# Optimization experiments

Hardware: AMD Instinct MI355X
Metric: run time of the kernel (lower is better)

The kernel has to match this reference:

```python
import jax, jax.numpy as jnp
import numpy as np

HID = 256; H2 = 512; EMB = 128
B, K, NR, LR, LQ, NQ = 16, 4, 5, 100, 60, 5
VOCAB, EXTRA = 50000, 100
EPS = 1e-12


def setup_inputs() -> dict:
    key = jax.random.key(0)
    ks = jax.random.split(key, 32)
    n = lambda k, s, sc=1.0: jax.random.normal(k, s, jnp.float32) * sc
    W = 0.02
    return {
        'y_t': n(ks[0], (B, EMB)),
        'h0': n(ks[1], (B, HID)),
        'c0': n(ks[2], (B, HID)),
        'c_t_0': n(ks[3], (B, H2)),
        'o_m': n(ks[4], (B, H2 + EMB)),
        'h_q': n(ks[5], (B, NQ, LQ, H2)),
        'q_mask': jnp.ones((B, LQ), jnp.float32),
        'q_a': n(ks[6], (B, NQ, EMB)),
        'h_r': n(ks[7], (B, K, NR, LR, H2)),
        'r_mask': jnp.ones((B, K, LR), jnp.float32),
        'r_a': n(ks[8], (B, K, NR, EMB)),
        'r_o': n(ks[9], (B, K, NR, EMB)),
        'qr_cov': jnp.zeros((B, LQ + K * LR), jnp.float32),
        'extra_zeros': jnp.zeros((B, EXTRA), jnp.float32),
        'xc_w': n(ks[10], (EMB, EMB + H2), W),
        'xc_b': jnp.zeros((EMB,), jnp.float32),
        'w_ih': n(ks[11], (4 * HID, EMB), W),
        'w_hh': n(ks[12], (4 * HID, HID), W),
        'b_ih': jnp.zeros((4 * HID,), jnp.float32),
        'b_hh': jnp.zeros((4 * HID,), jnp.float32),
        'dsq_w': n(ks[13], (H2, EMB), W),
        'dsa_w': n(ks[14], (H2 + EMB, EMB), W),
        'dso_w': n(ks[15], (2 * H2 + EMB, EMB), W),
        'U_w': n(ks[16], (H2, H2), W),
        'Wc_w': n(ks[17], (H2,), W),
        'Ws_w': n(ks[18], (H2, H2), W),
        'Wqr_w': n(ks[19], (H2, H2), W),
        'Wqr_b': jnp.zeros((H2,), jnp.float32),
        'Vr_w': n(ks[20], (H2,), W),
        'pg_w': n(ks[21], (2 * H2,), W),
        'pg_b': jnp.zeros((), jnp.float32),
        'pv1_w': n(ks[22], (H2, 2 * H2), W),
        'pv1_b': jnp.zeros((H2,), jnp.float32),
        'pv2_w': n(ks[23], (VOCAB, H2), W),
        'pv2_b': jnp.zeros((VOCAB,), jnp.float32),
        'batch_extend_vocab': jax.random.randint(ks[24], (B, LQ + K * LR), 0, VOCAB + EXTRA),
        'step': 1,
    }


def dynamic_select(W, s_t, h_s, s_a):
    # s_t: [b, D]; h_s: [b, n, l, h]; s_a: [b, n, e]; bilinear -> tanh -> sum-normalize
    w = jnp.tanh(jnp.einsum('bd,de,bne->bn', s_t, W, s_a))
    w = w / (w.sum(axis=1, keepdims=True) + EPS)
    w_h_s = jnp.einsum('bn,bnlh->blh', w, h_s)
    w_a = jnp.einsum('bn,bne->be', w, s_a)
    return w_h_s, w_a


def decoder_attention(U_w, Wc_w, Ws_w, Wqr_w, Wqr_b, Vr_w, h_q, q_mask, h_r, r_mask, s_t, qr_cov):
    # h_q: [b,l_q,h]; h_r: [b,k,l_r,h]
    b, l_q, h = h_q.shape
    k, l_r = h_r.shape[1], h_r.shape[2]
    qU = h_q @ U_w.T                                        # [b,l_q,h]
    U = jnp.tanh(jnp.einsum('bqh,bkrh->bkqr', qU, h_r))      # [b,k,l_q,l_r]
    alpha_q = jax.nn.softmax(U.max(axis=3), axis=-1)         # [b,k,l_q]
    alpha_r = jax.nn.softmax(U.max(axis=2), axis=-1)         # [b,k,l_r]
    pai_q = jnp.einsum('bkq,bq,bqh->bqh', alpha_q, q_mask, h_q) / k   # mean over k
    pai_r = ((alpha_r * r_mask)[..., None] * h_r).reshape(b, k * l_r, h)
    pai = jnp.concatenate([pai_q, pai_r], axis=1)            # [b, L, h]
    dec_fea = (s_t @ Ws_w.T)[:, None, :] + pai @ Wqr_w.T + Wqr_b + qr_cov[..., None] * Wc_w
    e = jnp.tanh(dec_fea) @ Vr_w                             # [b, L]
    mask = jnp.concatenate([q_mask, r_mask.reshape(b, k * l_r)], axis=1)
    a = jax.nn.softmax(e, axis=1) * mask
    a = a / a.sum(axis=1, keepdims=True)
    c_t = jnp.einsum('bl,blh->bh', a, pai)
    return c_t, a, qr_cov + a


def reference(y_t, h0, c0, c_t_0, o_m, h_q, q_mask, q_a, h_r, r_mask, r_a, r_o, qr_cov,
              extra_zeros, xc_w, xc_b, w_ih, w_hh, b_ih, b_hh, dsq_w, dsa_w, dso_w,
              U_w, Wc_w, Ws_w, Wqr_w, Wqr_b, Vr_w, pg_w, pg_b, pv1_w, pv1_b, pv2_w, pv2_b,
              batch_extend_vocab, step):
    b, k, n_r, l_r, h = h_r.shape
    # input projection + 1-step LSTM (PyTorch gate order i,f,g,o)
    x = jnp.concatenate([y_t, c_t_0], axis=1) @ xc_w.T + xc_b
    gates = x @ w_ih.T + b_ih + h0 @ w_hh.T + b_hh
    i, f, g, o = jnp.split(gates, 4, axis=1)
    c1 = jax.nn.sigmoid(f) * c0 + jax.nn.sigmoid(i) * jnp.tanh(g)
    h1 = jax.nn.sigmoid(o) * jnp.tanh(c1)
    s_t_hat = jnp.concatenate([h1, c1], axis=1)             # [b, 2*hid]
    # dynamic selections
    q_t, q_a_t = dynamic_select(dsq_w, s_t_hat, h_q, q_a)   # [b,l_q,h], [b,d]
    s_a_t = jnp.concatenate([
        jnp.broadcast_to(s_t_hat[:, None, :], (b, k, h)),
        jnp.broadcast_to(q_a_t[:, None, :], (b, k, q_a_t.shape[-1]))], axis=2).reshape(b * k, -1)
    h_a_t, _ = dynamic_select(dsa_w, s_a_t, h_r.reshape(b * k, n_r, l_r, h), r_a.reshape(b * k, n_r, -1))
    s_o_t = jnp.concatenate([
        jnp.broadcast_to(s_t_hat[:, None, :], (b, k, h)),
        jnp.broadcast_to(o_m[:, None, :], (b, k, o_m.shape[-1]))], axis=2).reshape(b * k, -1)
    h_o_t, _ = dynamic_select(dso_w, s_o_t, h_r.reshape(b * k, n_r, l_r, h), r_o.reshape(b * k, n_r, -1))
    r_t = (h_a_t + h_o_t).reshape(b, k, l_r, h)
    # multi-source co-attention with coverage
    c_t, alpha_qr, qr_cov_next = decoder_attention(U_w, Wc_w, Ws_w, Wqr_w, Wqr_b, Vr_w,
                                                   q_t, q_mask, r_t, r_mask, s_t_hat, qr_cov)
    h_s_t = jnp.concatenate([s_t_hat, c_t], axis=-1)        # [b, 4*hid]
    p_gen = jax.nn.sigmoid(h_s_t @ pg_w + pg_b)[:, None]    # [b,1]
    hid = h_s_t @ pv1_w.T + pv1_b
    p_v = jax.nn.softmax(hid @ pv2_w.T + pv2_b, axis=1)     # [b, vocab]
    vocab_dist = jnp.concatenate([p_gen * p_v, extra_zeros], axis=1)
    attn_dist = (1.0 - p_gen) * alpha_qr
    rows = jnp.arange(b)[:, None]
    final_dist = vocab_dist.at[rows, batch_extend_vocab].add(attn_dist)
    return final_dist, h1, c1, c_t, alpha_qr, qr_cov_next
```

## Files before the change

### kernel.cpp

```cpp
#include <hip/hip_runtime.h>
#include <math.h>

#define BB 16
#define H2N 512
#define VOCABN 50000
#define EXTRAN 100
#define LTOT 460
#define EPSF 1e-12f

__device__ __forceinline__ float sigm(float x){ return 1.0f/(1.0f+expf(-x)); }

__device__ __forceinline__ float wred(float v){
  #pragma unroll
  for (int s=32;s>0;s>>=1) v += __shfl_xor(v,s);
  return v;
}
__device__ __forceinline__ float wredmax(float v){
  #pragma unroll
  for (int s=32;s>0;s>>=1) v = fmaxf(v, __shfl_xor(v,s));
  return v;
}

__global__ __launch_bounds__(256) void k_w4(
    const float* __restrict__ A, const float* __restrict__ B,
    float* __restrict__ A4, float* __restrict__ B4)
{
  int idx = blockIdx.x*256 + threadIdx.x;
  int m = idx >> 16;
  int r = idx & 65535;
  int k4 = r >> 9;
  int h  = r & 511;
  const float* src = m ? B : A;
  float* dst = m ? B4 : A4;
  float4 v = *(const float4*)(src + (long)h*512 + k4*4);
  *(float4*)(dst + (long)k4*2048 + h*4) = v;
}

__global__ __launch_bounds__(1024) void k_head(
    const float* __restrict__ y_t, const float* __restrict__ h0, const float* __restrict__ c0,
    const float* __restrict__ c_t_0, const float* __restrict__ o_m,
    const float* __restrict__ q_a, const float* __restrict__ r_a, const float* __restrict__ r_o,
    const float* __restrict__ xc_w, const float* __restrict__ xc_b,
    const float* __restrict__ w_ih, const float* __restrict__ w_hh,
    const float* __restrict__ b_ih, const float* __restrict__ b_hh,
    const float* __restrict__ dsq_w, const float* __restrict__ dsa_w, const float* __restrict__ dso_w,
    const float* __restrict__ Ws_w,
    float* __restrict__ sthat, float* __restrict__ out_h1, float* __restrict__ out_c1,
    float* __restrict__ wq_o, float* __restrict__ cw_o, float* __restrict__ WsS_o)
{
  __shared__ float cat[640], h0s[256], xls[128], gs[1024];
  __shared__ float s[512], om[640], qa_l[640];
  __shared__ float part[1024];
  __shared__ float tq[128], ta[128], to2[128];
  __shared__ float wr2[20], wal[20], sums[4], wql[8], scal[4];
  int b = blockIdx.x, t = threadIdx.x;
  int w = t>>6, lane = t&63;

  if (t < 640){
    cat[t] = (t<128) ? y_t[b*128+t] : c_t_0[b*512 + (t-128)];
    om[t]  = o_m[b*640+t];
    qa_l[t]= q_a[b*640+t];
  } else if (t < 896){
    h0s[t-640] = h0[b*256 + (t-640)];
  }
  __syncthreads();

  {
    int j0 = w*8;
    for (int i=0;i<8;++i){
      int j = j0+i;
      const float* row = xc_w + j*640;
      float a = 0.f;
      #pragma unroll
      for (int it=0; it<10; ++it) a += cat[lane+64*it]*row[lane+64*it];
      a = wred(a);
      if (lane==0) xls[j] = a + xc_b[j];
    }
  }
  __syncthreads();

  {
    int r0 = w*64;
    for (int i=0;i<64;++i){
      int r = r0+i;
      const float* wi = w_ih + r*128;
      const float* wh = w_hh + r*256;
      float a = xls[lane]*wi[lane] + xls[lane+64]*wi[lane+64];
      #pragma unroll
      for (int it=0; it<4; ++it) a += h0s[lane+64*it]*wh[lane+64*it];
      a = wred(a);
      if (lane==0) gs[r] = a + b_ih[r] + b_hh[r];
    }
  }
  __syncthreads();

  if (t < 256){
    float c1v = sigm(gs[256+t])*c0[b*256+t] + sigm(gs[t])*tanhf(gs[512+t]);
    float h1v = sigm(gs[768+t])*tanhf(c1v);
    s[t] = h1v; s[256+t] = c1v;
    sthat[b*512+t] = h1v; sthat[b*512+256+t] = c1v;
    out_h1[b*256+t] = h1v; out_c1[b*256+t] = c1v;
  }
  __syncthreads();

  {
    int j = t&127, seg = t>>7, d0 = seg*64;
    float a = 0.f;
    #pragma unroll 8
    for (int it=0; it<64; ++it){ int d = d0+it; a += s[d]*dsq_w[d*128+j]; }
    part[seg*128+j] = a;
  }
  __syncthreads();
  if (t < 128){
    float a = 0.f;
    #pragma unroll
    for (int sg=0; sg<8; ++sg) a += part[sg*128+t];
    tq[t] = a;
  }
  __syncthreads();

  if (w < 5){
    float p = tq[lane]*qa_l[w*128+lane] + tq[lane+64]*qa_l[w*128+64+lane];
    p = wred(p);
    if (lane==0) wr2[w] = tanhf(p);
  }
  __syncthreads();
  if (t==0){ float sm=EPSF; for(int n=0;n<5;++n) sm+=wr2[n]; scal[0]=sm; }
  __syncthreads();
  if (t<5){ float v = wr2[t]/scal[0]; wql[t]=v; wq_o[b*5+t]=v; }
  __syncthreads();
  if (t<128){
    float a=0.f;
    #pragma unroll
    for (int n=0;n<5;++n) a += wql[n]*qa_l[n*128+t];
    tq[t]=a;
  }
  __syncthreads();

  {
    int j = t&127, seg = t>>7, d0 = seg*80;
    float a = 0.f;
    for (int it=0; it<80; ++it){
      int d = d0+it;
      float sv = (d<512) ? s[d] : tq[d-512];
      a += sv*dsa_w[d*128+j];
    }
    part[seg*128+j] = a;
  }
  __syncthreads();
  if (t < 128){
    float a=0.f;
    #pragma unroll
    for (int sg=0; sg<8; ++sg) a += part[sg*128+t];
    ta[t]=a;
  }
  __syncthreads();

  for (int oo=w; oo<20; oo+=16){
    const float* ra = r_a + ((long)(b*4 + oo/5)*5 + (oo%5))*128;
    float p = ta[lane]*ra[lane] + ta[lane+64]*ra[lane+64];
    p = wred(p);
    if (lane==0) wr2[oo] = tanhf(p);
  }
  __syncthreads();
  if (t<4){ float sm=EPSF; for(int n=0;n<5;++n) sm+=wr2[t*5+n]; sums[t]=sm; }
  __syncthreads();
  if (t<20) wal[t] = wr2[t]/sums[t/5];
  __syncthreads();

  {
    int j = t&127, seg = t>>7, d0 = seg*144;
    float a = 0.f;
    for (int it=0; it<144; ++it){
      int d = d0+it;
      float sv = (d<512) ? s[d] : om[d-512];
      a += sv*dso_w[d*128+j];
    }
    part[seg*128+j] = a;
  }
  __syncthreads();
  if (t < 128){
    float a=0.f;
    #pragma unroll
    for (int sg=0; sg<8; ++sg) a += part[sg*128+t];
    to2[t]=a;
  }
  __syncthreads();

  for (int oo=w; oo<20; oo+=16){
    const float* ro = r_o + ((long)(b*4 + oo/5)*5 + (oo%5))*128;
    float p = to2[lane]*ro[lane] + to2[lane+64]*ro[lane+64];
    p = wred(p);
    if (lane==0) wr2[oo] = tanhf(p);
  }
  __syncthreads();
  if (t<4){ float sm=EPSF; for(int n=0;n<5;++n) sm+=wr2[t*5+n]; sums[t]=sm; }
  __syncthreads();
  if (t<20) cw_o[b*20+t] = wal[t] + wr2[t]/sums[t/5];

  for (int i=0;i<32;++i){
    int h = w*32 + i;
    const float* row = Ws_w + (long)h*512;
    float a = 0.f;
    #pragma unroll
    for (int it=0; it<8; ++it) a += s[lane+64*it]*row[lane+64*it];
    a = wred(a);
    if (lane==0) WsS_o[b*512+h] = a;
  }
}

#define NQT4 (BB*60*128)
__global__ __launch_bounds__(256) void k_wsum(
    const float* __restrict__ h_q, const float* __restrict__ h_r,
    const float* __restrict__ wq, const float* __restrict__ cw,
    float* __restrict__ q_t, float* __restrict__ r_t)
{
  __shared__ float cf[5];
  long idx = (long)blockIdx.x*256 + threadIdx.x;
  if (blockIdx.x < 480) {
    int b = (int)(idx / (60*128));
    if (threadIdx.x < 5) cf[threadIdx.x] = wq[b*5+threadIdx.x];
    __syncthreads();
    int rem = (int)(idx % (60*128));
    int l = rem/128, h4 = rem&127;
    const float4* src = (const float4*)h_q;
    float4 acc = {0,0,0,0};
    #pragma unroll
    for (int n=0;n<5;++n){
      float4 v = src[(((long)(b*5+n)*60 + l)<<7) + h4];
      float ww = cf[n];
      acc.x += ww*v.x; acc.y += ww*v.y; acc.z += ww*v.z; acc.w += ww*v.w;
    }
    ((float4*)q_t)[((long)(b*60+l)<<7) + h4] = acc;
  } else {
    long j = idx - NQT4;
    int bk = (int)(j / (100*128));
    if (threadIdx.x < 5) cf[threadIdx.x] = cw[bk*5+threadIdx.x];
    __syncthreads();
    int rem = (int)(j % (100*128));
    int l = rem/128, h4 = rem&127;
    const float4* src = (const float4*)h_r;
// ... 8 lines not shown
  }
}

__global__ __launch_bounds__(256) void k_qU(
    const float* __restrict__ q_t, const float* __restrict__ U4, float* __restrict__ qU)
{
  __shared__ float qt[4*512];
  int bid = blockIdx.x;
  int b = bid / 30; int r2 = bid % 30; int tile = r2 >> 1; int half = r2 & 1;
  int q0 = tile*4; int C0 = half*256;
  int t = threadIdx.x;
  {
    const float4* src = (const float4*)(q_t + (long)(b*60+q0)*512);
    ((float4*)qt)[t]     = src[t];
    ((float4*)qt)[t+256] = src[t+256];
  }
  __syncthreads();
  int c0 = t&63, rg = t>>6;
  float acc[4] = {};
  #pragma unroll 2
  for (int k4=0; k4<128; ++k4){
    float4 p = *(const float4*)&qt[rg*512 + k4*4];
    #pragma unroll
    for (int m=0;m<4;++m){
      float4 wv = *(const float4*)(U4 + (long)k4*2048 + (C0 + c0 + 64*m)*4);
      acc[m] += p.x*wv.x + p.y*wv.y + p.z*wv.z + p.w*wv.w;
    }
  }
  #pragma unroll
  for (int m=0;m<4;++m)
    qU[(long)(b*60+q0+rg)*512 + C0 + c0 + 64*m] = acc[m];
}

__global__ __launch_bounds__(1024) void k_umax(
    const float* __restrict__ qU, const float* __restrict__ r_t,
    float* __restrict__ aq, float* __restrict__ ar)
{
  __shared__ float qb[4*60*33];
  __shared__ float rb[4*100*33];
  __shared__ float C[6000];
  __shared__ float uq[60], ur[100], scal[4];
  int bid = blockIdx.x; int b = bid>>2, k = bid&3, t = threadIdx.x;
  int g = t>>8, u = t&255;
  bool act = u < 255;
  int tq = u/17, tr = u%17;
  int q0 = tq*4, r0 = tr*6;
  int nv = (r0+6<=100)? 6 : (100-r0);
  float acc[4][6] = {};
  const float* qbase = qU + (long)b*60*512;
  const float* rbase = r_t + (long)(b*4+k)*100*512;
  float* qg = qb + g*60*33;
  float* rg = rb + g*100*33;
  for (int cc=0; cc<4; ++cc){
    int k0 = (g*4+cc)*32;
    for (int i=u; i<60*32; i+=256){ int q=i>>5, hh=i&31; qg[q*33+hh] = qbase[(long)q*512 + k0 + hh]; }
    for (int i=u; i<100*32; i+=256){ int r=i>>5, hh=i&31; rg[r*33+hh] = rbase[(long)r*512 + k0 + hh]; }
    __syncthreads();
    if (act){
      for (int hh=0; hh<32; ++hh){
        float a0=qg[(q0+0)*33+hh], a1=qg[(q0+1)*33+hh], a2=qg[(q0+2)*33+hh], a3=qg[(q0+3)*33+hh];
        #pragma unroll
        for (int j=0;j<6;++j){
          float rv = rg[(r0+j)*33+hh];
          acc[0][j]+=a0*rv; acc[1][j]+=a1*rv; acc[2][j]+=a2*rv; acc[3][j]+=a3*rv;
        }
      }
    }
    __syncthreads();
  }
  for (int gi=0; gi<4; ++gi){
    if (g==gi && act){
      #pragma unroll
      for (int i=0;i<4;++i)
        for (int j=0;j<6;++j) if (j<nv){
          int cell = (q0+i)*100 + (r0+j);
          if (gi==0) C[cell] = acc[i][j];
          else       C[cell] += acc[i][j];
        }
    }
    __syncthreads();
  }
  if (t<60){
    float m=-1e30f;
    for (int i=0;i<100;++i) m = fmaxf(m, C[t*100+i]);
    uq[t] = tanhf(m);
  } else if (t>=64 && t<164){
    int rr = t-64;
    float m=-1e30f;
    for (int q=0;q<60;++q) m = fmaxf(m, C[q*100+rr]);
    ur[rr] = tanhf(m);
  }
  __syncthreads();
  if (t==0){ float M=-1e30f; for(int q=0;q<60;++q) M=fmaxf(M,uq[q]); scal[0]=M; }
  if (t==64){ float M=-1e30f; for(int r=0;r<100;++r) M=fmaxf(M,ur[r]); scal[1]=M; }
  __syncthreads();
  if (t<60) uq[t]=expf(uq[t]-scal[0]);
  if (t>=64&&t<164) ur[t-64]=expf(ur[t-64]-scal[1]);
  __syncthreads();
  if (t==0){ float S=0; for(int q=0;q<60;++q)S+=uq[q]; scal[2]=S; }
  if (t==64){ float S=0; for(int r=0;r<100;++r)S+=ur[r]; scal[3]=S; }
  __syncthreads();
  if (t<60) aq[(long)bid*60 + t] = uq[t]/scal[2];
  if (t>=64&&t<164) ar[(long)bid*100 + (t-64)] = ur[t-64]/scal[3];
}

__global__ __launch_bounds__(256) void k_proj_e(
    const float* __restrict__ q_t, const float* __restrict__ r_t,
    const float* __restrict__ aq, const float* __restrict__ ar,
    const float* __restrict__ q_mask, const float* __restrict__ r_mask,
    const float* __restrict__ W4, const float* __restrict__ Wqr_b,
    const float* __restrict__ Wc_w, const float* __restrict__ Vr_w,
    const float* __restrict__ WsS, const float* __restrict__ qr_cov,
    float* __restrict__ e_o)
{
  __shared__ float pt[16*512];
  __shared__ float cov[16], coef[16];
  int bid = blockIdx.x;
  int b = bid / 58; int r2 = bid % 58; int tile = r2 >> 1; int half = r2 & 1;
  int l0 = tile*16; int C0 = half*256;
  int t = threadIdx.x;
  int nrows = (460-l0 < 16)? (460-l0) : 16;
  if (t<16){
    float pc=0.f, cv=0.f;
    if (t<nrows){
      int l = l0+t;
      cv = qr_cov[b*460+l];
      if (l < 60){
        float s4 = aq[(b*4+0)*60+l]+aq[(b*4+1)*60+l]+aq[(b*4+2)*60+l]+aq[(b*4+3)*60+l];
        pc = s4 * q_mask[b*60+l] * 0.25f;
      } else {
        pc = ar[b*400+(l-60)] * r_mask[b*400+(l-60)];
      }
    }
    coef[t]=pc; cov[t]=cv;
  }
  __syncthreads();
// ... 17 lines not shown
    float4 wv[4];
    #pragma unroll
    for (int m=0;m<4;++m)
      wv[m] = *(const float4*)(W4 + (long)k4*2048 + (C0 + c0 + 64*m)*4);
    #pragma unroll
    for (int r=0;r<4;++r){
      float4 p = *(const float4*)&pt[(r0+r)*512 + k4*4];
      #pragma unroll
      for (int m=0;m<4;++m)
        acc[r][m] += p.x*wv[m].x + p.y*wv[m].y + p.z*wv[m].z + p.w*wv[m].w;
    }
  }
  float wsm[4], wbm[4], wcm[4], vrm[4];
  #pragma unroll
  for (int m=0;m<4;++m){
    int h = C0 + c0 + 64*m;
    wsm[m] = WsS[b*512+h]; wbm[m] = Wqr_b[h];
    wcm[m] = Wc_w[h];      vrm[m] = Vr_w[h];
  }
  int lane = t&63;
  #pragma unroll
  for (int r=0;r<4;++r){
    int row = r0+r;
    float cv = cov[row];
    float s = 0.f;
    #pragma unroll
    for (int m=0;m<4;++m)
      s += tanhf(wsm[m] + acc[r][m] + wbm[m] + cv*wcm[m]) * vrm[m];
    s = wred(s);
    if (lane==0 && row<nrows) atomicAdd(&e_o[b*460+l0+row], s);
  }
}

__global__ __launch_bounds__(1024) void k_attnfin(
    const float* __restrict__ e_i, const float* __restrict__ q_mask, const float* __restrict__ r_mask,
    const float* __restrict__ qr_cov,
    const float* __restrict__ q_t, const float* __restrict__ r_t,
    const float* __restrict__ aq, const float* __restrict__ ar,
    const float* __restrict__ sthat, const float* __restrict__ pg_w, const float* __restrict__ pg_b,
    const float* __restrict__ pv1_w, const float* __restrict__ pv1_b,
    float* __restrict__ a_o, float* __restrict__ hid_o, float* __restrict__ pgen_o,
    float* __restrict__ out_ct, float* __restrict__ out_a, float* __restrict__ out_cov)
{
  __shared__ float aL[460], coefL[460], hst[1024], parts[1024], red[16];
  int b = blockIdx.x, t = threadIdx.x, w = t>>6, lane = t&63;
  if (t<512) hst[t] = sthat[b*512+t];
  float ev = (t<460) ? e_i[b*460+t] : -1e30f;
  float m = wredmax(ev);
  if (lane==0) red[w]=m;
  __syncthreads();
  float M=-1e30f;
  #pragma unroll
  for (int i=0;i<16;++i) M=fmaxf(M,red[i]);
  __syncthreads();
  float x = 0.f;
  if (t<460){
    float mk = (t<60) ? q_mask[b*60+t] : r_mask[b*400+(t-60)];
    x = expf(ev-M)*mk;
  }
  float sr = wred(x);
  if (lane==0) red[w]=sr;
  __syncthreads();
  float S=0.f;
  #pragma unroll
  for (int i=0;i<16;++i) S+=red[i];
  __syncthreads();
  if (t<460){
    float v = x/S;
    aL[t]=v;
    a_o[b*460+t]=v; out_a[b*460+t]=v; out_cov[b*460+t]=qr_cov[b*460+t]+v;
    float pc;
    if (t<60){
      float s4 = aq[(b*4+0)*60+t]+aq[(b*4+1)*60+t]+aq[(b*4+2)*60+t]+aq[(b*4+3)*60+t];
      pc = s4 * q_mask[b*60+t] * 0.25f;
    } else {
      pc = ar[b*400+(t-60)] * r_mask[b*400+(t-60)];
    }
    coefL[t]=v*pc;
  }
  __syncthreads();
  {
    int h = t&511, seg = t>>9;
    float a0 = 0.f, a1 = 0.f;
    int lA = seg*230;
    #pragma unroll 4
    for (int i=0; i<230; i+=2){
      int l1 = lA+i, l2 = lA+i+1;
      const float* s1 = (l1<60) ? (q_t + ((long)(b*60+l1)<<9))
                                : (r_t + ((long)(b*400+(l1-60))<<9));
      const float* s2 = (l2<60) ? (q_t + ((long)(b*60+l2)<<9))
                                : (r_t + ((long)(b*400+(l2-60))<<9));
      a0 += coefL[l1]*s1[h];
      a1 += coefL[l2]*s2[h];
    }
    parts[t]=a0+a1;
  }
  __syncthreads();
  if (t<512){
    float ct = parts[t]+parts[512+t];
    hst[512+t]=ct;
    out_ct[b*512+t]=ct;
  }
  __syncthreads();
  {
    float p = hst[t]*pg_w[t];
    p = wred(p);
    if (lane==0) red[w]=p;
  }
  __syncthreads();
  if (t==0){
    float pp = pg_b[0];
    #pragma unroll
    for (int i=0;i<16;++i) pp+=red[i];
    pgen_o[b]=sigm(pp);
  }
  for (int i=0;i<32;++i){
    int h = w*32+i;
    const float* row = pv1_w + (long)h*1024;
    float a = 0.f;
    #pragma unroll
    for (int it=0; it<16; ++it) a += hst[lane+64*it]*row[lane+64*it];
    a = wred(a);
    if (lane==0) hid_o[b*512+h] = a + pv1_b[h];
  }
}

__global__ __launch_bounds__(256) void k_logits(
    const float* __restrict__ hid, const float* __restrict__ pv2_w, const float* __restrict__ pv2_b,
    float* __restrict__ logits, float* __restrict__ S)
{
  __shared__ float hs[16*512];
  __shared__ float ssum[16];
  int t = threadIdx.x;
  for (int i=t;i<8192;i+=256) hs[i]=hid[i];
  if (t<16) ssum[t]=0.f;
  __syncthreads();
  int vl = t>>2, seg = t&3;
  long v = (long)blockIdx.x*64 + vl;
  float acc[16]={};
  if (v < VOCABN){
    const float4* wr = (const float4*)(pv2_w + v*512 + seg*128);
    const float4* hv = ((const float4*)hs) + seg*32;
    for (int i=0;i<32;++i){
      int j = (i + seg*2)&31;
      float4 wv = wr[j];
      #pragma unroll
      for (int b2=0;b2<16;++b2){
        float4 h = hv[b2*128+j];
        acc[b2] += wv.x*h.x+wv.y*h.y+wv.z*h.z+wv.w*h.w;
      }
    }
  }
  #pragma unroll
  for (int b2=0;b2<16;++b2){
    acc[b2] += __shfl_xor(acc[b2],1);
    acc[b2] += __shfl_xor(acc[b2],2);
// ... 61 lines not shown
  const float* xc_w  = (const float*)d_in[14];
  const float* xc_b  = (const float*)d_in[15];
  const float* w_ih  = (const float*)d_in[16];
  const float* w_hh  = (const float*)d_in[17];
  const float* b_ih  = (const float*)d_in[18];
  const float* b_hh  = (const float*)d_in[19];
  const float* dsq_w = (const float*)d_in[20];
  const float* dsa_w = (const float*)d_in[21];
  const float* dso_w = (const float*)d_in[22];
  const float* U_w   = (const float*)d_in[23];
  const float* Wc_w  = (const float*)d_in[24];
  const float* Ws_w  = (const float*)d_in[25];
  const float* Wqr_w = (const float*)d_in[26];
  const float* Wqr_b = (const float*)d_in[27];
  const float* Vr_w  = (const float*)d_in[28];
  const float* pg_w  = (const float*)d_in[29];
  const float* pg_b  = (const float*)d_in[30];
  const float* pv1_w = (const float*)d_in[31];
  const float* pv1_b = (const float*)d_in[32];
  const float* pv2_w = (const float*)d_in[33];
  const float* pv2_b = (const float*)d_in[34];
  const int*   bev   = (const int*)d_in[35];

  float* out = (float*)d_out;
  float* out_fd  = out;
  float* out_h1  = out_fd + (size_t)16*(VOCABN+EXTRAN);
  float* out_c1  = out_h1 + 16*256;
  float* out_ct  = out_c1 + 16*256;
  float* out_a   = out_ct + 16*512;
  float* out_cov = out_a  + 16*460;

  float* ws = (float*)d_ws;
  size_t o = 0;
  float* sthat = ws + o; o += 16*512;
  float* wq    = ws + o; o += 16*8;
  float* cw    = ws + o; o += 16*32;
  float* WsS   = ws + o; o += 16*512;
  float* U4    = ws + o; o += (size_t)512*512;
  float* Wqr4  = ws + o; o += (size_t)512*512;
  float* q_t   = ws + o; o += (size_t)16*60*512;
  float* r_t   = ws + o; o += (size_t)16*400*512;
  float* qU    = ws + o; o += (size_t)16*60*512;
  float* aq    = ws + o; o += 16*4*64;
  float* ar    = ws + o; o += 16*4*112;
  float* e_b   = ws + o; o += 16*512;
  float* a_b   = ws + o; o += 16*512;
  float* hid_b = ws + o; o += 16*512;
  float* pgen  = ws + o; o += 64;
  float* Ssum  = ws + o; o += 64;
  float* logits= ws + o; o += (size_t)16*VOCABN;

  hipMemsetAsync(e_b, 0, 16*512*sizeof(float), stream);
  hipMemsetAsync(Ssum, 0, 64*sizeof(float), stream);

  hipLaunchKernelGGL(k_w4, dim3(512), dim3(256), 0, stream, U_w, Wqr_w, U4, Wqr4);
  hipLaunchKernelGGL(k_head, dim3(16), dim3(1024), 0, stream,
      y_t,h0,c0,c_t_0,o_m,q_a,r_a,r_o,
      xc_w,xc_b,w_ih,w_hh,b_ih,b_hh,dsq_w,dsa_w,dso_w,Ws_w,
      sthat,out_h1,out_c1, wq,cw,WsS);
  hipLaunchKernelGGL(k_wsum, dim3(3680), dim3(256), 0, stream,
      h_q,h_r,wq,cw, q_t,r_t);
  hipLaunchKernelGGL(k_qU, dim3(480), dim3(256), 0, stream, q_t, U4, qU);
  hipLaunchKernelGGL(k_umax, dim3(64), dim3(1024), 0, stream, qU, r_t, aq, ar);
  hipLaunchKernelGGL(k_proj_e, dim3(928), dim3(256), 0, stream,
      q_t,r_t,aq,ar,q_mask,r_mask,Wqr4,Wqr_b,Wc_w,Vr_w,WsS,qr_cov, e_b);
  hipLaunchKernelGGL(k_attnfin, dim3(16), dim3(1024), 0, stream,
      e_b,q_mask,r_mask,qr_cov,q_t,r_t,aq,ar,sthat,pg_w,pg_b,pv1_w,pv1_b,
      a_b,hid_b,pgen, out_ct,out_a,out_cov);
  hipLaunchKernelGGL(k_logits, dim3((VOCABN+63)/64), dim3(256), 0, stream,
      hid_b, pv2_w, pv2_b, logits, Ssum);
  hipLaunchKernelGGL(k_scale, dim3((16*(VOCABN+EXTRAN)+255)/256), dim3(256), 0, stream,
      logits, extra_zeros, pgen, Ssum, out_fd);
  hipLaunchKernelGGL(k_scatter, dim3(16), dim3(512), 0, stream,
      a_b, pgen, bev, out_fd);
}
```

Before: 684.1 us.

## Split serial per-batch head and attention kernels into many-block batched kernels

The monolithic 16-block head kernel (LSTM, dynamic-select projections, Ws projection) is split into several kernels that process all 16 batch rows per weight row, spreading the weight reads over many blocks. Partial projections are combined with atomics into a buffer that is zeroed once with a single memset. The score-max kernel is retiled across 128 blocks with 64-wide K chunks and a separate softmax kernel, and the final attention kernel is split into softmax, context-sum, p_gen and hidden-projection kernels with more blocks. The cost is more kernel launches and atomic adds in exchange for far more parallelism on the small serial stages.

```diff
diff --git a/kernel.cpp b/kernel.cpp
--- a/kernel.cpp
+++ b/kernel.cpp
@@ -2,7 +2,6 @@
 #include <math.h>
 
 #define BB 16
-#define H2N 512
 #define VOCABN 50000
 #define EXTRAN 100
 #define LTOT 460
@@ -36,177 +35,209 @@
   *(float4*)(dst + (long)k4*2048 + h*4) = v;
 }
 
-__global__ __launch_bounds__(1024) void k_head(
-    const float* __restrict__ y_t, const float* __restrict__ h0, const float* __restrict__ c0,
-    const float* __restrict__ c_t_0, const float* __restrict__ o_m,
-    const float* __restrict__ q_a, const float* __restrict__ r_a, const float* __restrict__ r_o,
+__global__ __launch_bounds__(256) void k_xl(
+    const float* __restrict__ y_t, const float* __restrict__ c_t_0,
     const float* __restrict__ xc_w, const float* __restrict__ xc_b,
+    float* __restrict__ xls)
+{
+  __shared__ float cat[16*640];
+  int t = threadIdx.x, w = t>>6, lane = t&63;
+  for (int i=t;i<16*640;i+=256){
+    int b2=i/640, d=i%640;
+    cat[i] = (d<128)? y_t[b2*128+d] : c_t_0[b2*512 + d-128];
+  }
+  __syncthreads();
+  int j = blockIdx.x*4 + w;
+  const float* row = xc_w + (long)j*640;
+  float acc[16]={};
+  #pragma unroll
+  for (int i=0;i<10;++i){
+    float wv = row[lane+64*i];
+    #pragma unroll
+    for (int b2=0;b2<16;++b2) acc[b2] += wv*cat[b2*640 + lane+64*i];
+  }
+  float bias = xc_b[j];
+  #pragma unroll
+  for (int b2=0;b2<16;++b2){
+    float v = wred(acc[b2]);
+    if (lane==0) xls[b2*128+j] = v + bias;
+  }
+}
+
+__global__ __launch_bounds__(256) void k_gates(
+    const float* __restrict__ xls, const float* __restrict__ h0,
     const float* __restrict__ w_ih, const float* __restrict__ w_hh,
     const float* __restrict__ b_ih, const float* __restrict__ b_hh,
-    const float* __restrict__ dsq_w, const float* __restrict__ dsa_w, const float* __restrict__ dso_w,
+    float* __restrict__ gates)
+{
+  __shared__ float xh[16*384];
+  int t = threadIdx.x, w = t>>6, lane = t&63;
+  for (int i=t;i<16*384;i+=256){
+    int b2=i/384, d=i%384;
+    xh[i] = (d<128)? xls[b2*128+d] : h0[b2*256 + d-128];
+  }
+  __syncthreads();
+  int r = blockIdx.x*4 + w;
+  float acc[16]={};
+  #pragma unroll
+  for (int i=0;i<2;++i){
+    float wv = w_ih[(long)r*128 + lane + 64*i];
+    #pragma unroll
+    for (int b2=0;b2<16;++b2) acc[b2] += wv*xh[b2*384 + lane+64*i];
+  }
+  #pragma unroll
+  for (int i=0;i<4;++i){
+    float wv = w_hh[(long)r*256 + lane + 64*i];
+    #pragma unroll
+    for (int b2=0;b2<16;++b2) acc[b2] += wv*xh[b2*384 + 128 + lane+64*i];
+  }
+  float bias = b_ih[r]+b_hh[r];
+  #pragma unroll
+  for (int b2=0;b2<16;++b2){
+    float v = wred(acc[b2]);
+    if (lane==0) gates[b2*1024 + r] = v + bias;
+  }
+}
+
+__global__ __launch_bounds__(256) void k_cell(
+    const float* __restrict__ gates, const float* __restrict__ c0,
+    float* __restrict__ sthat, float* __restrict__ out_h1, float* __restrict__ out_c1)
+{
+  int b = blockIdx.x, t = threadIdx.x;
+  float gi = gates[b*1024+t], gf = gates[b*1024+256+t];
+  float gg = gates[b*1024+512+t], go = gates[b*1024+768+t];
+  float c1v = sigm(gf)*c0[b*256+t] + sigm(gi)*tanhf(gg);
+  float h1v = sigm(go)*tanhf(c1v);
+  sthat[b*512+t] = h1v; sthat[b*512+256+t] = c1v;
+  out_h1[b*256+t] = h1v; out_c1[b*256+t] = c1v;
+}
+
+__global__ __launch_bounds__(128) void k_tmpq(
+    const float* __restrict__ sthat, const float* __restrict__ dsq_w,
+    float* __restrict__ tmpq)
+{
+  __shared__ float sseg[64];
+  int bid = blockIdx.x; int b = bid>>3, seg = bid&7;
+  int d0 = seg*64, t = threadIdx.x;
+  if (t<64) sseg[t] = sthat[b*512 + d0 + t];
+  __syncthreads();
+  float acc = 0.f;
+  for (int d=0;d<64;++d) acc += sseg[d]*dsq_w[(long)(d0+d)*128 + t];
+  atomicAdd(&tmpq[b*128+t], acc);
+}
+
+__global__ __launch_bounds__(128) void k_wq(
+    const float* __restrict__ tmpq, const float* __restrict__ q_a,
+    float* __restrict__ wq_o, float* __restrict__ qat)
+{
+  __shared__ float tq[128], qa_l[640], wr2[5], wql[5], scal[1];
+  int b = blockIdx.x, t = threadIdx.x;
+  tq[t] = tmpq[b*128+t];
+  for (int i=t;i<640;i+=128) qa_l[i] = q_a[b*640+i];
+  __syncthreads();
+  if (t<5){
+    float p=0.f;
+    for (int e2=0;e2<128;++e2) p += tq[e2]*qa_l[t*128+e2];
+    wr2[t]=tanhf(p);
+  }
+  __syncthreads();
+  if (t==0){ float sm=EPSF; for(int n=0;n<5;++n) sm+=wr2[n]; scal[0]=sm; }
+  __syncthreads();
+  if (t<5){ float v = wr2[t]/scal[0]; wql[t]=v; wq_o[b*5+t]=v; }
+  __syncthreads();
+  float a=0.f;
+  #pragma unroll
+  for (int n=0;n<5;++n) a += wql[n]*qa_l[n*128+t];
+  qat[b*128+t]=a;
+}
+
+__global__ __launch_bounds__(256) void k_mix(
+    const float* __restrict__ sthat, const float* __restrict__ qat,
+    const float* __restrict__ o_m,
+    const float* __restrict__ dsa_w, const float* __restrict__ dso_w,
     const float* __restrict__ Ws_w,
-    float* __restrict__ sthat, float* __restrict__ out_h1, float* __restrict__ out_c1,
-    float* __restrict__ wq_o, float* __restrict__ cw_o, float* __restrict__ WsS_o)
-{
-  __shared__ float cat[640], h0s[256], xls[128], gs[1024];
-  __shared__ float s[512], om[640], qa_l[640];
-  __shared__ float part[1024];
-  __shared__ float tq[128], ta[128], to2[128];
-  __shared__ float wr2[20], wal[20], sums[4], wql[8], scal[4];
-  int b = blockIdx.x, t = threadIdx.x;
-  int w = t>>6, lane = t&63;
-
-  if (t < 640){
-    cat[t] = (t<128) ? y_t[b*128+t] : c_t_0[b*512 + (t-128)];
-    om[t]  = o_m[b*640+t];
-    qa_l[t]= q_a[b*640+t];
-  } else if (t < 896){
-    h0s[t-640] = h0[b*256 + (t-640)];
-  }
-  __syncthreads();
-
-  {
-    int j0 = w*8;
+    float* __restrict__ tmpa, float* __restrict__ tmpo, float* __restrict__ WsS)
+{
+  __shared__ float smem[8192];
+  int bid = blockIdx.x, t = threadIdx.x;
+  if (bid < 128){
+    int b = bid>>3, seg = bid&7, d0 = seg*80;
+    if (t<80){
+      int d = d0+t;
+      smem[t] = (d<512)? sthat[b*512+d] : qat[b*128 + d-512];
+    }
+    __syncthreads();
+    int j = t&127, half = t>>7;
+    float acc=0.f;
+    for (int dd=0;dd<40;++dd){
+      int d = half*40+dd;
+      acc += smem[d]*dsa_w[(long)(d0+d)*128 + j];
+    }
+    atomicAdd(&tmpa[b*128+j], acc);
+  } else if (bid < 256){
+    int idx = bid-128; int b = idx>>3, seg = idx&7, d0 = seg*144;
+    for (int i=t;i<144;i+=256){
+      int d = d0+i;
+      smem[i] = (d<512)? sthat[b*512+d] : o_m[b*640 + d-512];
+    }
+    __syncthreads();
+    int j = t&127, half = t>>7;
+    float acc=0.f;
+    for (int dd=0;dd<72;++dd){
+      int d = half*72+dd;
+      acc += smem[d]*dso_w[(long)(d0+d)*128 + j];
+    }
+    atomicAdd(&tmpo[b*128+j], acc);
+  } else {
+    int idx = bid-256;
+    int w = t>>6, lane = t&63;
+    for (int i=t;i<8192;i+=256){
+      smem[i] = sthat[i];
+    }
+    __syncthreads();
+    int h = idx*4 + w;
+    const float* row = Ws_w + (long)h*512;
+    float acc[16]={};
+    #pragma unroll
     for (int i=0;i<8;++i){
-      int j = j0+i;
-      const float* row = xc_w + j*640;
-      float a = 0.f;
+      float wv = row[lane+64*i];
       #pragma unroll
-      for (int it=0; it<10; ++it) a += cat[lane+64*it]*row[lane+64*it];
-      a = wred(a);
-      if (lane==0) xls[j] = a + xc_b[j];
-    }
-  }
-  __syncthreads();
-
-  {
-    int r0 = w*64;
-    for (int i=0;i<64;++i){
-      int r = r0+i;
-      const float* wi = w_ih + r*128;
-      const float* wh = w_hh + r*256;
-      float a = xls[lane]*wi[lane] + xls[lane+64]*wi[lane+64];
-      #pragma unroll
-      for (int it=0; it<4; ++it) a += h0s[lane+64*it]*wh[lane+64*it];
-      a = wred(a);
-      if (lane==0) gs[r] = a + b_ih[r] + b_hh[r];
-    }
-  }
-  __syncthreads();
-
-  if (t < 256){
-    float c1v = sigm(gs[256+t])*c0[b*256+t] + sigm(gs[t])*tanhf(gs[512+t]);
-    float h1v = sigm(gs[768+t])*tanhf(c1v);
-    s[t] = h1v; s[256+t] = c1v;
-    sthat[b*512+t] = h1v; sthat[b*512+256+t] = c1v;
-    out_h1[b*256+t] = h1v; out_c1[b*256+t] = c1v;
-  }
-  __syncthreads();
-
-  {
-    int j = t&127, seg = t>>7, d0 = seg*64;
-    float a = 0.f;
-    #pragma unroll 8
-    for (int it=0; it<64; ++it){ int d = d0+it; a += s[d]*dsq_w[d*128+j]; }
-    part[seg*128+j] = a;
-  }
-  __syncthreads();
-  if (t < 128){
-    float a = 0.f;
-    #pragma unroll
-    for (int sg=0; sg<8; ++sg) a += part[sg*128+t];
-    tq[t] = a;
-  }
-  __syncthreads();
-
-  if (w < 5){
-    float p = tq[lane]*qa_l[w*128+lane] + tq[lane+64]*qa_l[w*128+64+lane];
-    p = wred(p);
-    if (lane==0) wr2[w] = tanhf(p);
-  }
-  __syncthreads();
-  if (t==0){ float sm=EPSF; for(int n=0;n<5;++n) sm+=wr2[n]; scal[0]=sm; }
-  __syncthreads();
-  if (t<5){ float v = wr2[t]/scal[0]; wql[t]=v; wq_o[b*5+t]=v; }
-  __syncthreads();
-  if (t<128){
-    float a=0.f;
-    #pragma unroll
-    for (int n=0;n<5;++n) a += wql[n]*qa_l[n*128+t];
-    tq[t]=a;
-  }
-  __syncthreads();
-
-  {
-    int j = t&127, seg = t>>7, d0 = seg*80;
-    float a = 0.f;
-    for (int it=0; it<80; ++it){
-      int d = d0+it;
-      float sv = (d<512) ? s[d] : tq[d-512];
-      a += sv*dsa_w[d*128+j];
-    }
-    part[seg*128+j] = a;
-  }
-  __syncthreads();
-  if (t < 128){
-    float a=0.f;
-    #pragma unroll
-    for (int sg=0; sg<8; ++sg) a += part[sg*128+t];
-    ta[t]=a;
-  }
-  __syncthreads();
-
-  for (int oo=w; oo<20; oo+=16){
-    const float* ra = r_a + ((long)(b*4 + oo/5)*5 + (oo%5))*128;
-    float p = ta[lane]*ra[lane] + ta[lane+64]*ra[lane+64];
-    p = wred(p);
-    if (lane==0) wr2[oo] = tanhf(p);
-  }
-  __syncthreads();
-  if (t<4){ float sm=EPSF; for(int n=0;n<5;++n) sm+=wr2[t*5+n]; sums[t]=sm; }
-  __syncthreads();
-  if (t<20) wal[t] = wr2[t]/sums[t/5];
-  __syncthreads();
-
-  {
-    int j = t&127, seg = t>>7, d0 = seg*144;
-    float a = 0.f;
-    for (int it=0; it<144; ++it){
-      int d = d0+it;
-      float sv = (d<512) ? s[d] : om[d-512];
-      a += sv*dso_w[d*128+j];
-    }
-    part[seg*128+j] = a;
-  }
-  __syncthreads();
-  if (t < 128){
-    float a=0.f;
-    #pragma unroll
-    for (int sg=0; sg<8; ++sg) a += part[sg*128+t];
-    to2[t]=a;
-  }
-  __syncthreads();
-
-  for (int oo=w; oo<20; oo+=16){
-    const float* ro = r_o + ((long)(b*4 + oo/5)*5 + (oo%5))*128;
-    float p = to2[lane]*ro[lane] + to2[lane+64]*ro[lane+64];
-    p = wred(p);
-    if (lane==0) wr2[oo] = tanhf(p);
-  }
-  __syncthreads();
-  if (t<4){ float sm=EPSF; for(int n=0;n<5;++n) sm+=wr2[t*5+n]; sums[t]=sm; }
-  __syncthreads();
-  if (t<20) cw_o[b*20+t] = wal[t] + wr2[t]/sums[t/5];
-
-  for (int i=0;i<32;++i){
-    int h = w*32 + i;
-    const float* row = Ws_w + (long)h*512;
-    float a = 0.f;
-    #pragma unroll
-    for (int it=0; it<8; ++it) a += s[lane+64*it]*row[lane+64*it];
-    a = wred(a);
-    if (lane==0) WsS_o[b*512+h] = a;
-  }
+      for (int b2=0;b2<16;++b2) acc[b2] += wv*smem[b2*512 + lane+64*i];
+    }
+    #pragma unroll
+    for (int b2=0;b2<16;++b2){
+      float v = wred(acc[b2]);
+      if (lane==0) WsS[b2*512+h] = v;
+    }
+  }
+}
+
+__global__ __launch_bounds__(256) void k_cw(
+    const float* __restrict__ tmpa, const float* __restrict__ tmpo,
+    const float* __restrict__ r_a, const float* __restrict__ r_o,
+    float* __restrict__ cw_o)
+{
+  __shared__ float ta[128], to[128], wra[20], wro[20], sa[4], so[4];
+  int b = blockIdx.x, t = threadIdx.x, w = t>>6, lane = t&63;
+  if (t<128) ta[t]=tmpa[b*128+t];
+  else if (t<256) to[t-128]=tmpo[b*128+(t-128)];
+  __syncthreads();
+  for (int oo=w; oo<20; oo+=4){
+    const float* ra = r_a + ((long)(b*20+oo))*128;
+    const float* ro = r_o + ((long)(b*20+oo))*128;
+    float pa = ta[lane]*ra[lane] + ta[lane+64]*ra[lane+64];
+    float po = to[lane]*ro[lane] + to[lane+64]*ro[lane+64];
+    pa = wred(pa); po = wred(po);
+    if (lane==0){ wra[oo]=tanhf(pa); wro[oo]=tanhf(po); }
+  }
+  __syncthreads();
+  if (t<4){
+    float s1=EPSF, s2=EPSF;
+    for (int n=0;n<5;++n){ s1+=wra[t*5+n]; s2+=wro[t*5+n]; }
+    sa[t]=s1; so[t]=s2;
+  }
+  __syncthreads();
+  if (t<20) cw_o[b*20+t] = wra[t]/sa[t/5] + wro[t]/so[t/5];
 }
 
 #define NQT4 (BB*60*128)
@@ -281,76 +312,98 @@
     qU[(long)(b*60+q0+rg)*512 + C0 + c0 + 64*m] = acc[m];
 }
 
-__global__ __launch_bounds__(1024) void k_umax(
+__global__ __launch_bounds__(256) void k_sc(
     const float* __restrict__ qU, const float* __restrict__ r_t,
-    float* __restrict__ aq, float* __restrict__ ar)
-{
-  __shared__ float qb[4*60*33];
-  __shared__ float rb[4*100*33];
-  __shared__ float C[6000];
-  __shared__ float uq[60], ur[100], scal[4];
-  int bid = blockIdx.x; int b = bid>>2, k = bid&3, t = threadIdx.x;
-  int g = t>>8, u = t&255;
-  bool act = u < 255;
-  int tq = u/17, tr = u%17;
-  int q0 = tq*4, r0 = tr*6;
-  int nv = (r0+6<=100)? 6 : (100-r0);
-  float acc[4][6] = {};
+    float* __restrict__ mqp, float* __restrict__ mrp)
+{
+  __shared__ float qs[64*65];
+  __shared__ float rs[64*65];
+  __shared__ float mqb[60*16];
+  __shared__ float mrb[52*16];
+  int bid = blockIdx.x;
+  int b = bid>>3, k = (bid>>1)&3, half = bid&1;
+  int t = threadIdx.x;
   const float* qbase = qU + (long)b*60*512;
-  const float* rbase = r_t + (long)(b*4+k)*100*512;
-  float* qg = qb + g*60*33;
-  float* rg = rb + g*100*33;
-  for (int cc=0; cc<4; ++cc){
-    int k0 = (g*4+cc)*32;
-    for (int i=u; i<60*32; i+=256){ int q=i>>5, hh=i&31; qg[q*33+hh] = qbase[(long)q*512 + k0 + hh]; }
-    for (int i=u; i<100*32; i+=256){ int r=i>>5, hh=i&31; rg[r*33+hh] = rbase[(long)r*512 + k0 + hh]; }
+  const float* rbase = r_t + ((long)(b*4+k)*100 + half*50)*512;
+  int tq = t&15, tr = t>>4;
+  int q0 = tq*4, r0 = tr*4;
+  int nq = (q0<60)? ((60-q0<4)?(60-q0):4) : 0;
+  int nr = (r0<50)? ((50-r0<4)?(50-r0):4) : 0;
+  float acc[4][4]={};
+  for (int c=0;c<8;++c){
+    int k0 = c*64;
+    for (int i=t;i<60*64;i+=256){ int q=i>>6, kk=i&63; qs[q*65+kk]=qbase[(long)q*512+k0+kk]; }
+    for (int i=t;i<50*64;i+=256){ int r=i>>6, kk=i&63; rs[r*65+kk]=rbase[(long)r*512+k0+kk]; }
     __syncthreads();
-    if (act){
-      for (int hh=0; hh<32; ++hh){
-        float a0=qg[(q0+0)*33+hh], a1=qg[(q0+1)*33+hh], a2=qg[(q0+2)*33+hh], a3=qg[(q0+3)*33+hh];
-        #pragma unroll
-        for (int j=0;j<6;++j){
-          float rv = rg[(r0+j)*33+hh];
-          acc[0][j]+=a0*rv; acc[1][j]+=a1*rv; acc[2][j]+=a2*rv; acc[3][j]+=a3*rv;
-        }
-      }
-    }
-    __syncthreads();
-  }
-  for (int gi=0; gi<4; ++gi){
-    if (g==gi && act){
+    for (int kk=0;kk<64;++kk){
+      float qv[4], rv[4];
+      #pragma unroll
+      for (int i=0;i<4;++i) qv[i]=qs[(q0+i)*65+kk];
+      #pragma unroll
+      for (int j=0;j<4;++j) rv[j]=rs[(r0+j)*65+kk];
       #pragma unroll
       for (int i=0;i<4;++i)
-        for (int j=0;j<6;++j) if (j<nv){
-          int cell = (q0+i)*100 + (r0+j);
-          if (gi==0) C[cell] = acc[i][j];
-          else       C[cell] += acc[i][j];
-        }
+        #pragma unroll
+        for (int j=0;j<4;++j) acc[i][j]+=qv[i]*rv[j];
     }
     __syncthreads();
   }
+  if (nr>0){
+    #pragma unroll
+    for (int i=0;i<4;++i) if (i<nq){
+      float m=-1e30f;
+      #pragma unroll
+      for (int j=0;j<4;++j) if (j<nr) m=fmaxf(m,acc[i][j]);
+      mqb[(q0+i)*16+tr]=m;
+    }
+  }
+  if (nq>0){
+    #pragma unroll
+    for (int j=0;j<4;++j) if (j<nr){
+      float m=-1e30f;
+      #pragma unroll
+      for (int i=0;i<4;++i) if (i<nq) m=fmaxf(m,acc[i][j]);
+      mrb[(r0+j)*16+tq]=m;
+    }
+  }
+  __syncthreads();
   if (t<60){
     float m=-1e30f;
-    for (int i=0;i<100;++i) m = fmaxf(m, C[t*100+i]);
+    for (int jj=0;jj<13;++jj) m=fmaxf(m,mqb[t*16+jj]);
+    mqp[(long)bid*60 + t] = m;
+  } else if (t>=64 && t<114){
+    int rr=t-64;
+    float m=-1e30f;
+    for (int jj=0;jj<15;++jj) m=fmaxf(m,mrb[rr*16+jj]);
+    mrp[((long)(b*4+k))*100 + half*50 + rr] = m;
+  }
+}
+
+__global__ __launch_bounds__(128) void k_alpha(
+    const float* __restrict__ mqp, const float* __restrict__ mrp,
+    float* __restrict__ aq, float* __restrict__ ar)
+{
+  __shared__ float uq[60], ur[100], scal[4];
+  int bid = blockIdx.x, t = threadIdx.x;
+  if (t<60){
+    float m = fmaxf(mqp[(long)(bid*2)*60+t], mqp[(long)(bid*2+1)*60+t]);
     uq[t] = tanhf(m);
-  } else if (t>=64 && t<164){
-    int rr = t-64;
-    float m=-1e30f;
-    for (int q=0;q<60;++q) m = fmaxf(m, C[q*100+rr]);
-    ur[rr] = tanhf(m);
-  }
-  __syncthreads();
-  if (t==0){ float M=-1e30f; for(int q=0;q<60;++q) M=fmaxf(M,uq[q]); scal[0]=M; }
-  if (t==64){ float M=-1e30f; for(int r=0;r<100;++r) M=fmaxf(M,ur[r]); scal[1]=M; }
-  __syncthreads();
-  if (t<60) uq[t]=expf(uq[t]-scal[0]);
-  if (t>=64&&t<164) ur[t-64]=expf(ur[t-64]-scal[1]);
-  __syncthreads();
-  if (t==0){ float S=0; for(int q=0;q<60;++q)S+=uq[q]; scal[2]=S; }
-  if (t==64){ float S=0; for(int r=0;r<100;++r)S+=ur[r]; scal[3]=S; }
-  __syncthreads();
-  if (t<60) aq[(long)bid*60 + t] = uq[t]/scal[2];
-  if (t>=64&&t<164) ar[(long)bid*100 + (t-64)] = ur[t-64]/scal[3];
+  }
+  if (t<100) ur[t] = tanhf(mrp[(long)bid*100+t]);
+  __syncthreads();
+  if (t==0){
+    float M=-1e30f; for (int q=0;q<60;++q) M=fmaxf(M,uq[q]);
+    float S=0.f;    for (int q=0;q<60;++q) S+=expf(uq[q]-M);
+    scal[0]=M; scal[2]=S;
+  }
+  if (t==64){
+    float M=-1e30f; for (int r=0;r<100;++r) M=fmaxf(M,ur[r]);
+    float S=0.f;    for (int r=0;r<100;++r) S+=expf(ur[r]-M);
+    scal[1]=M; scal[3]=S;
+  }
+  __syncthreads();
+  if (t<60)  aq[(long)bid*60+t]  = expf(uq[t]-scal[0])/scal[2];
+  if (t<100) ar[(long)bid*100+t] = expf(ur[t]-scal[1])/scal[3];
 }
 
 __global__ __launch_bounds__(256) void k_proj_e(
@@ -434,26 +487,22 @@
   }
 }
 
-__global__ __launch_bounds__(1024) void k_attnfin(
-    const float* __restrict__ e_i, const float* __restrict__ q_mask, const float* __restrict__ r_mask,
-    const float* __restrict__ qr_cov,
-    const float* __restrict__ q_t, const float* __restrict__ r_t,
+__global__ __launch_bounds__(512) void k_smax(
+    const float* __restrict__ e_i, const float* __restrict__ q_mask,
+    const float* __restrict__ r_mask, const float* __restrict__ qr_cov,
     const float* __restrict__ aq, const float* __restrict__ ar,
-    const float* __restrict__ sthat, const float* __restrict__ pg_w, const float* __restrict__ pg_b,
-    const float* __restrict__ pv1_w, const float* __restrict__ pv1_b,
-    float* __restrict__ a_o, float* __restrict__ hid_o, float* __restrict__ pgen_o,
-    float* __restrict__ out_ct, float* __restrict__ out_a, float* __restrict__ out_cov)
-{
-  __shared__ float aL[460], coefL[460], hst[1024], parts[1024], red[16];
+    float* __restrict__ a_o, float* __restrict__ coef_o,
+    float* __restrict__ out_a, float* __restrict__ out_cov)
+{
+  __shared__ float red[8];
   int b = blockIdx.x, t = threadIdx.x, w = t>>6, lane = t&63;
-  if (t<512) hst[t] = sthat[b*512+t];
-  float ev = (t<460) ? e_i[b*460+t] : -1e30f;
+  float ev = (t<460)? e_i[b*460+t] : -1e30f;
   float m = wredmax(ev);
   if (lane==0) red[w]=m;
   __syncthreads();
   float M=-1e30f;
   #pragma unroll
-  for (int i=0;i<16;++i) M=fmaxf(M,red[i]);
+  for (int i=0;i<8;++i) M=fmaxf(M,red[i]);
   __syncthreads();
   float x = 0.f;
   if (t<460){
@@ -465,11 +514,9 @@
   __syncthreads();
   float S=0.f;
   #pragma unroll
-  for (int i=0;i<16;++i) S+=red[i];
-  __syncthreads();
+  for (int i=0;i<8;++i) S+=red[i];
   if (t<460){
     float v = x/S;
-    aL[t]=v;
     a_o[b*460+t]=v; out_a[b*460+t]=v; out_cov[b*460+t]=qr_cov[b*460+t]+v;
     float pc;
     if (t<60){
@@ -478,52 +525,75 @@
     } else {
       pc = ar[b*400+(t-60)] * r_mask[b*400+(t-60)];
     }
-    coefL[t]=v*pc;
-  }
-  __syncthreads();
-  {
-    int h = t&511, seg = t>>9;
-    float a0 = 0.f, a1 = 0.f;
-    int lA = seg*230;
-    #pragma unroll 4
-    for (int i=0; i<230; i+=2){
-      int l1 = lA+i, l2 = lA+i+1;
-      const float* s1 = (l1<60) ? (q_t + ((long)(b*60+l1)<<9))
-                                : (r_t + ((long)(b*400+(l1-60))<<9));
-      const float* s2 = (l2<60) ? (q_t + ((long)(b*60+l2)<<9))
-                                : (r_t + ((long)(b*400+(l2-60))<<9));
-      a0 += coefL[l1]*s1[h];
-      a1 += coefL[l2]*s2[h];
-    }
-    parts[t]=a0+a1;
-  }
-  __syncthreads();
-  if (t<512){
-    float ct = parts[t]+parts[512+t];
-    hst[512+t]=ct;
-    out_ct[b*512+t]=ct;
-  }
-  __syncthreads();
-  {
-    float p = hst[t]*pg_w[t];
-    p = wred(p);
-    if (lane==0) red[w]=p;
-  }
-  __syncthreads();
-  if (t==0){
-    float pp = pg_b[0];
-    #pragma unroll
-    for (int i=0;i<16;++i) pp+=red[i];
-    pgen_o[b]=sigm(pp);
-  }
-  for (int i=0;i<32;++i){
-    int h = w*32+i;
-    const float* row = pv1_w + (long)h*1024;
-    float a = 0.f;
-    #pragma unroll
-    for (int it=0; it<16; ++it) a += hst[lane+64*it]*row[lane+64*it];
-    a = wred(a);
-    if (lane==0) hid_o[b*512+h] = a + pv1_b[h];
+    coef_o[b*460+t]=v*pc;
+  }
+}
+
+__global__ __launch_bounds__(256) void k_ct(
+    const float* __restrict__ coef_o, const float* __restrict__ q_t,
+    const float* __restrict__ r_t, float* __restrict__ ct)
+{
+  __shared__ float cf[58];
+  int bid = blockIdx.x; int b = bid>>3, seg = bid&7;
+  int l0 = seg*58; int ln = (460-l0<58)? (460-l0):58;
+  int t = threadIdx.x;
+  if (t<ln) cf[t]=coef_o[b*460+l0+t];
+  __syncthreads();
+  float a0=0.f, a1=0.f;
+  for (int i=0;i<ln;++i){
+    int l = l0+i;
+    const float2* src = (l<60)? (const float2*)(q_t + ((long)(b*60+l)<<9))
+                              : (const float2*)(r_t + ((long)(b*400+(l-60))<<9));
+    float2 v = src[t];
+    a0 += cf[i]*v.x; a1 += cf[i]*v.y;
+  }
+  atomicAdd(&ct[b*512 + 2*t],   a0);
+  atomicAdd(&ct[b*512 + 2*t+1], a1);
+}
+
+__global__ __launch_bounds__(256) void k_pgen(
+    const float* __restrict__ sthat, const float* __restrict__ ct,
+    const float* __restrict__ pg_w, const float* __restrict__ pg_b,
+    float* __restrict__ pgen_o, float* __restrict__ out_ct)
+{
+  __shared__ float red[4];
+  int b = blockIdx.x, t = threadIdx.x, lane = t&63, w = t>>6;
+  float c1 = ct[b*512+t], c2 = ct[b*512+256+t];
+  out_ct[b*512+t]=c1; out_ct[b*512+256+t]=c2;
+  float p = sthat[b*512+t]*pg_w[t] + sthat[b*512+256+t]*pg_w[256+t]
+          + c1*pg_w[512+t] + c2*pg_w[768+t];
+  p = wred(p);
+  if (lane==0) red[w]=p;
+  __syncthreads();
+  if (t==0) pgen_o[b]=sigm(red[0]+red[1]+red[2]+red[3]+pg_b[0]);
+}
+
+__global__ __launch_bounds__(256) void k_hid(
+    const float* __restrict__ sthat, const float* __restrict__ ct,
+    const float* __restrict__ pv1_w, const float* __restrict__ pv1_b,
+    float* __restrict__ hid)
+{
+  __shared__ float hst[16*1024];
+  int t = threadIdx.x, w = t>>6, lane = t&63;
+  for (int i=t;i<16*1024;i+=256){
+    int b2=i>>10, d=i&1023;
+    hst[i] = (d<512)? sthat[b2*512+d] : ct[b2*512 + d-512];
+  }
+  __syncthreads();
+  int h = blockIdx.x*4 + w;
+  const float* row = pv1_w + (long)h*1024;
+  float acc[16]={};
+  #pragma unroll
+  for (int i=0;i<16;++i){
+    float wv = row[lane+64*i];
+    #pragma unroll
+    for (int b2=0;b2<16;++b2) acc[b2] += wv*hst[b2*1024 + lane+64*i];
+  }
+  float bias = pv1_b[h];
+  #pragma unroll
+  for (int b2=0;b2<16;++b2){
+    float v = wred(acc[b2]);
+    if (lane==0) hid[b2*512+h] = v + bias;
   }
 }
 
@@ -651,41 +721,62 @@
 
   float* ws = (float*)d_ws;
   size_t o = 0;
-  float* sthat = ws + o; o += 16*512;
-  float* wq    = ws + o; o += 16*8;
-  float* cw    = ws + o; o += 16*32;
-  float* WsS   = ws + o; o += 16*512;
+  float* zbase = ws + o;
+  float* tmpq  = ws + o; o += 2048;
+  float* tmpa  = ws + o; o += 2048;
+  float* tmpo  = ws + o; o += 2048;
+  float* e_b   = ws + o; o += 7360;
+  float* ct    = ws + o; o += 8192;
+  float* Ssum  = ws + o; o += 64;
+  size_t zcount = o;
+  float* sthat = ws + o; o += 8192;
+  float* xls   = ws + o; o += 2048;
+  float* gates = ws + o; o += 16384;
+  float* wq    = ws + o; o += 128;
+  float* qat   = ws + o; o += 2048;
+  float* cw    = ws + o; o += 512;
+  float* WsS   = ws + o; o += 8192;
   float* U4    = ws + o; o += (size_t)512*512;
   float* Wqr4  = ws + o; o += (size_t)512*512;
   float* q_t   = ws + o; o += (size_t)16*60*512;
   float* r_t   = ws + o; o += (size_t)16*400*512;
   float* qU    = ws + o; o += (size_t)16*60*512;
-  float* aq    = ws + o; o += 16*4*64;
-  float* ar    = ws + o; o += 16*4*112;
-  float* e_b   = ws + o; o += 16*512;
-  float* a_b   = ws + o; o += 16*512;
-  float* hid_b = ws + o; o += 16*512;
+  float* aq    = ws + o; o += 3840;
+  float* ar    = ws + o; o += 6400;
+  float* mqp   = ws + o; o += 7680;
+  float* mrp   = ws + o; o += 6400;
+  float* coefb = ws + o; o += 7360;
+  float* a_b   = ws + o; o += 7360;
+  float* hid_b = ws + o; o += 8192;
   float* pgen  = ws + o; o += 64;
-  float* Ssum  = ws + o; o += 64;
   float* logits= ws + o; o += (size_t)16*VOCABN;
 
-  hipMemsetAsync(e_b, 0, 16*512*sizeof(float), stream);
-  hipMemsetAsync(Ssum, 0, 64*sizeof(float), stream);
-
+  hipMemsetAsync(zbase, 0, zcount*sizeof(float), stream);
   hipLaunchKernelGGL(k_w4, dim3(512), dim3(256), 0, stream, U_w, Wqr_w, U4, Wqr4);
-  hipLaunchKernelGGL(k_head, dim3(16), dim3(1024), 0, stream,
-      y_t,h0,c0,c_t_0,o_m,q_a,r_a,r_o,
-      xc_w,xc_b,w_ih,w_hh,b_ih,b_hh,dsq_w,dsa_w,dso_w,Ws_w,
-      sthat,out_h1,out_c1, wq,cw,WsS);
+  hipLaunchKernelGGL(k_xl, dim3(32), dim3(256), 0, stream, y_t, c_t_0, xc_w, xc_b, xls);
+  hipLaunchKernelGGL(k_gates, dim3(256), dim3(256), 0, stream,
+      xls, h0, w_ih, w_hh, b_ih, b_hh, gates);
+  hipLaunchKernelGGL(k_cell, dim3(16), dim3(256), 0, stream,
+      gates, c0, sthat, out_h1, out_c1);
+  hipLaunchKernelGGL(k_tmpq, dim3(128), dim3(128), 0, stream, sthat, dsq_w, tmpq);
+  hipLaunchKernelGGL(k_wq, dim3(16), dim3(128), 0, stream, tmpq, q_a, wq, qat);
+  hipLaunchKernelGGL(k_mix, dim3(384), dim3(256), 0, stream,
+      sthat, qat, o_m, dsa_w, dso_w, Ws_w, tmpa, tmpo, WsS);
+  hipLaunchKernelGGL(k_cw, dim3(16), dim3(256), 0, stream, tmpa, tmpo, r_a, r_o, cw);
   hipLaunchKernelGGL(k_wsum, dim3(3680), dim3(256), 0, stream,
-      h_q,h_r,wq,cw, q_t,r_t);
+      h_q, h_r, wq, cw, q_t, r_t);
   hipLaunchKernelGGL(k_qU, dim3(480), dim3(256), 0, stream, q_t, U4, qU);
-  hipLaunchKernelGGL(k_umax, dim3(64), dim3(1024), 0, stream, qU, r_t, aq, ar);
+  hipLaunchKernelGGL(k_sc, dim3(128), dim3(256), 0, stream, qU, r_t, mqp, mrp);
+  hipLaunchKernelGGL(k_alpha, dim3(64), dim3(128), 0, stream, mqp, mrp, aq, ar);
   hipLaunchKernelGGL(k_proj_e, dim3(928), dim3(256), 0, stream,
-      q_t,r_t,aq,ar,q_mask,r_mask,Wqr4,Wqr_b,Wc_w,Vr_w,WsS,qr_cov, e_b);
-  hipLaunchKernelGGL(k_attnfin, dim3(16), dim3(1024), 0, stream,
-      e_b,q_mask,r_mask,qr_cov,q_t,r_t,aq,ar,sthat,pg_w,pg_b,pv1_w,pv1_b,
-      a_b,hid_b,pgen, out_ct,out_a,out_cov);
+      q_t, r_t, aq, ar, q_mask, r_mask, Wqr4, Wqr_b, Wc_w, Vr_w, WsS, qr_cov, e_b);
+  hipLaunchKernelGGL(k_smax, dim3(16), dim3(512), 0, stream,
+      e_b, q_mask, r_mask, qr_cov, aq, ar, a_b, coefb, out_a, out_cov);
+  hipLaunchKernelGGL(k_ct, dim3(128), dim3(256), 0, stream, coefb, q_t, r_t, ct);
+  hipLaunchKernelGGL(k_pgen, dim3(16), dim3(256), 0, stream,
+      sthat, ct, pg_w, pg_b, pgen, out_ct);
+  hipLaunchKernelGGL(k_hid, dim3(128), dim3(256), 0, stream,
+      sthat, ct, pv1_w, pv1_b, hid_b);
   hipLaunchKernelGGL(k_logits, dim3((VOCABN+63)/64), dim3(256), 0, stream,
       hid_b, pv2_w, pv2_b, logits, Ssum);
   hipLaunchKernelGGL(k_scale, dim3((16*(VOCABN+EXTRAN)+255)/256), dim3(256), 0, stream,
```

Measured after the change: 600.0 us. -12.3%, faster.
